# Kernel optimization log

Measured on AMD Instinct MI355X. Metric: run time of the kernel, lower is better.

The kernel has to match this reference:

```python
import jax, jax.numpy as jnp
import numpy as np

B, N_PER, C, K = 64, 2048, 512, 512


def setup_inputs() -> dict:
    key = jax.random.key(0)
    k1, k2 = jax.random.split(key)
    feat0 = jax.random.normal(k1, (B * N_PER, C, 1), dtype=jnp.float32)
    # torch.randn(1, C) / sqrt(C)
    W = jax.random.normal(k2, (1, C), dtype=jnp.float32) / np.sqrt(C).astype(np.float32)
    return {"feat0": feat0, "W": W, "num_graphs": B, "nodes_per_graph": N_PER, "k": K}


def reference(feat0, W, num_graphs, nodes_per_graph, k):
    # feat0: [N, C, 1] degree-0 features, W: [1, C] projection weights
    Cdim = feat0.shape[1]
    # yi = (W @ feat) / ||W||  ->  one scalar score per node, shape [N, 1, 1]
    y = jnp.einsum('oc,nci->noi', W, feat0) / jnp.linalg.norm(W)
    yb = y.reshape(num_graphs, nodes_per_graph)  # [B, n] per-graph scores
    # descending top-k per graph (all graphs full -> no -inf padding needed)
    _, idx = jax.lax.top_k(yb, k)                 # [B, k] unsorted positions
    idx_sorted = jnp.sort(idx, axis=1)            # torch.sort(topk_indices, dim=1)
    # selected scores, shape [B*k, 1] (hidden_size = 1)
    y_sel = jnp.take_along_axis(yb, idx_sorted, axis=1).reshape(num_graphs * k, 1)
    # flattened node indices (equivalent to topk_indices_ with hidden_size=1)
    flat_idx = (idx_sorted + jnp.arange(num_graphs)[:, None] * nodes_per_graph).reshape(-1)
    feats_sel = feat0[flat_idx].reshape(num_graphs * k, Cdim)  # gather_row on xi
    # sigmoid gate and trailing unsqueeze -> [B*k, C, 1]
    out = (jax.nn.sigmoid(y_sel) * feats_sel)[..., None]
    return out, flat_idx
```

## Files before the change

### kernel.cpp

```cpp
#include <hip/hip_runtime.h>
#include <math.h>

#define NGRAPHS 64
#define NPER    2048
#define CDIM    512
#define KSEL    512
#define NNODES  (NGRAPHS * NPER)
#define NSEL    (NGRAPHS * KSEL)
#define OUT0    (NSEL * CDIM)

__global__ void norm_kernel(const float* __restrict__ W, float* __restrict__ invnorm) {
    __shared__ float red[512];
    int t = threadIdx.x;
    float w = W[t];
    red[t] = w * w;
    __syncthreads();
    for (int s = 256; s > 0; s >>= 1) {
        if (t < s) red[t] += red[t + s];
        __syncthreads();
    }
    if (t == 0) invnorm[0] = 1.0f / sqrtf(red[0]);
}

__global__ void scores_kernel(const float* __restrict__ feat,
                              const float* __restrict__ W,
                              float* __restrict__ scores) {
    int gtid = blockIdx.x * blockDim.x + threadIdx.x;
    int row  = gtid >> 6;
    int lane = threadIdx.x & 63;
    if (row >= NNODES) return;
    const float4* rowp = (const float4*)(feat + (size_t)row * CDIM);
    const float4* Wp   = (const float4*)W;
    float acc = 0.f;
#pragma unroll
    for (int p = 0; p < 2; ++p) {
        float4 f = rowp[lane + 64 * p];
        float4 w = Wp[lane + 64 * p];
        acc += f.x * w.x + f.y * w.y + f.z * w.z + f.w * w.w;
    }
#pragma unroll
    for (int off = 32; off > 0; off >>= 1) acc += __shfl_down(acc, off);
    if (lane == 0) scores[row] = acc;
}

__global__ void __launch_bounds__(1024) topk_kernel(const float* __restrict__ scores,
                                                    int* __restrict__ flatidx,
                                                    float* __restrict__ idx_out) {
    __shared__ float s[NPER];
    __shared__ int   id[NPER];
    int b = blockIdx.x;
    int t = threadIdx.x;
    const float* sb = scores + b * NPER;
    for (int i = t; i < NPER; i += 1024) { s[i] = sb[i]; id[i] = i; }
    __syncthreads();

    for (int k = 2; k <= NPER; k <<= 1) {
        for (int j = k >> 1; j > 0; j >>= 1) {
            int i = t + (t & ~(j - 1));
            int p = i | j;
            bool up = ((i & k) == 0);
            float si = s[i], sp = s[p];
            int   ii = id[i], ip = id[p];
            bool before = (si > sp) || (si == sp && ii < ip);
            if (up ? !before : before) {
                s[i] = sp; s[p] = si; id[i] = ip; id[p] = ii;
            }
            __syncthreads();
        }
    }

    for (int k = 2; k <= KSEL; k <<= 1) {
        for (int j = k >> 1; j > 0; j >>= 1) {
            if (t < KSEL / 2) {
                int i = t + (t & ~(j - 1));
                int p = i | j;
                bool up = ((i & k) == 0);
                int ii = id[i], ip = id[p];
                if (up ? (ii > ip) : (ii < ip)) { id[i] = ip; id[p] = ii; }
            }
            __syncthreads();
        }
    }

    if (t < KSEL) {
        int fi = b * NPER + id[t];
        flatidx[b * KSEL + t] = fi;
        idx_out[b * KSEL + t] = (float)fi;
    }
}

__global__ void gather_kernel(const float* __restrict__ feat,
                              const float* __restrict__ scores,
                              const float* __restrict__ invnorm,
                              const int* __restrict__ flatidx,
                              float* __restrict__ out) {
    int gtid = blockIdx.x * blockDim.x + threadIdx.x;
    int row  = gtid >> 6;
    int lane = threadIdx.x & 63;
    if (row >= NSEL) return;
    int fi = flatidx[row];
    float y = scores[fi] * invnorm[0];
    float g = 1.0f / (1.0f + expf(-y));
    const float4* src = (const float4*)(feat + (size_t)fi * CDIM);
    float4*       dst = (float4*)(out + (size_t)row * CDIM);
#pragma unroll
    for (int p = 0; p < 2; ++p) {
        float4 f = src[lane + 64 * p];
        f.x *= g; f.y *= g; f.z *= g; f.w *= g;
        dst[lane + 64 * p] = f;
    }
}

extern "C" void kernel_launch(void* const* d_in, const int* in_sizes, int n_in,
                              void* d_out, int out_size, void* d_ws, size_t ws_size,
                              hipStream_t stream) {
    const float* feat = (const float*)d_in[0];
    const float* W    = (const float*)d_in[1];
    float* out     = (float*)d_out;
    float* idx_out = out + OUT0;

    float* ws      = (float*)d_ws;
    float* scores  = ws;
    float* invnorm = ws + NNODES;
    int*   flatidx = (int*)(ws + NNODES + 64);

    norm_kernel  <<<1, 512, 0, stream>>>(W, invnorm);
    scores_kernel<<<NNODES / 4, 256, 0, stream>>>(feat, W, scores);
    topk_kernel  <<<NGRAPHS, 1024, 0, stream>>>(scores, flatidx, idx_out);
    gather_kernel<<<NSEL / 4, 256, 0, stream>>>(feat, scores, invnorm, flatidx, out);
}
```

Before: 415.9 us.

## Replace bitonic top-k with radix threshold select and fuse norm into scoring

The per-graph full bitonic sort of 2048 scores plus the index re-sort is replaced by a 32-step radix bisection on order-preserving float keys. It finds the k-th largest threshold, then uses prefix scans to emit selected indices already in ascending index order, with ties resolved by lowest index. The W norm is now computed inside each scoring warp instead of in a separate kernel, and the sigmoid gate is computed in top-k. Gather uses nontemporal stores and all kernels use larger blocks. Each scoring warp redundantly recomputes the norm, and the radix loop still needs two block barriers per bit.

```diff
diff --git a/kernel.cpp b/kernel.cpp
--- a/kernel.cpp
+++ b/kernel.cpp
@@ -9,105 +9,130 @@
 #define NSEL    (NGRAPHS * KSEL)
 #define OUT0    (NSEL * CDIM)
 
-__global__ void norm_kernel(const float* __restrict__ W, float* __restrict__ invnorm) {
-    __shared__ float red[512];
-    int t = threadIdx.x;
-    float w = W[t];
-    red[t] = w * w;
-    __syncthreads();
-    for (int s = 256; s > 0; s >>= 1) {
-        if (t < s) red[t] += red[t + s];
-        __syncthreads();
-    }
-    if (t == 0) invnorm[0] = 1.0f / sqrtf(red[0]);
-}
+typedef float floatx4 __attribute__((ext_vector_type(4)));
 
-__global__ void scores_kernel(const float* __restrict__ feat,
-                              const float* __restrict__ W,
-                              float* __restrict__ scores) {
+__global__ void __launch_bounds__(1024) scores_kernel(const float* __restrict__ feat,
+                                                      const float* __restrict__ W,
+                                                      float* __restrict__ nscores) {
     int gtid = blockIdx.x * blockDim.x + threadIdx.x;
     int row  = gtid >> 6;
     int lane = threadIdx.x & 63;
-    if (row >= NNODES) return;
     const float4* rowp = (const float4*)(feat + (size_t)row * CDIM);
     const float4* Wp   = (const float4*)W;
-    float acc = 0.f;
+    float acc = 0.f, wss = 0.f;
 #pragma unroll
     for (int p = 0; p < 2; ++p) {
         float4 f = rowp[lane + 64 * p];
         float4 w = Wp[lane + 64 * p];
         acc += f.x * w.x + f.y * w.y + f.z * w.z + f.w * w.w;
+        wss += w.x * w.x + w.y * w.y + w.z * w.z + w.w * w.w;
     }
 #pragma unroll
-    for (int off = 32; off > 0; off >>= 1) acc += __shfl_down(acc, off);
-    if (lane == 0) scores[row] = acc;
+    for (int off = 32; off; off >>= 1) {
+        acc += __shfl_down(acc, off);
+        wss += __shfl_down(wss, off);
+    }
+    if (lane == 0) nscores[row] = acc / sqrtf(wss);
 }
 
-__global__ void __launch_bounds__(1024) topk_kernel(const float* __restrict__ scores,
-                                                    int* __restrict__ flatidx,
-                                                    float* __restrict__ idx_out) {
-    __shared__ float s[NPER];
-    __shared__ int   id[NPER];
-    int b = blockIdx.x;
-    int t = threadIdx.x;
-    const float* sb = scores + b * NPER;
-    for (int i = t; i < NPER; i += 1024) { s[i] = sb[i]; id[i] = i; }
-    __syncthreads();
+__global__ void __launch_bounds__(512) topk_kernel(const float* __restrict__ nscores,
+                                                   int* __restrict__ flatidx,
+                                                   float* __restrict__ gate,
+                                                   float* __restrict__ idx_out) {
+    int b = blockIdx.x, t = threadIdx.x;
+    int lane = t & 63, wid = t >> 6;
+    const float* sb = nscores + b * NPER;
 
-    for (int k = 2; k <= NPER; k <<= 1) {
-        for (int j = k >> 1; j > 0; j >>= 1) {
-            int i = t + (t & ~(j - 1));
-            int p = i | j;
-            bool up = ((i & k) == 0);
-            float si = s[i], sp = s[p];
-            int   ii = id[i], ip = id[p];
-            bool before = (si > sp) || (si == sp && ii < ip);
-            if (up ? !before : before) {
-                s[i] = sp; s[p] = si; id[i] = ip; id[p] = ii;
-            }
-            __syncthreads();
-        }
+    float sc[4]; unsigned key[4];
+    float4 s4 = ((const float4*)sb)[t];
+    sc[0] = s4.x; sc[1] = s4.y; sc[2] = s4.z; sc[3] = s4.w;
+#pragma unroll
+    for (int e = 0; e < 4; ++e) {
+        unsigned u = __float_as_uint(sc[e]);
+        key[e] = (u & 0x80000000u) ? ~u : (u | 0x80000000u);
     }
 
-    for (int k = 2; k <= KSEL; k <<= 1) {
-        for (int j = k >> 1; j > 0; j >>= 1) {
-            if (t < KSEL / 2) {
-                int i = t + (t & ~(j - 1));
-                int p = i | j;
-                bool up = ((i & k) == 0);
-                int ii = id[i], ip = id[p];
-                if (up ? (ii > ip) : (ii < ip)) { id[i] = ip; id[p] = ii; }
-            }
-            __syncthreads();
+    __shared__ unsigned wred[8];
+    __shared__ unsigned bc;
+    unsigned prefix = 0u;
+    for (int bit = 31; bit >= 0; --bit) {
+        unsigned cand = prefix | (1u << bit);
+        int c = (key[0] >= cand) + (key[1] >= cand) + (key[2] >= cand) + (key[3] >= cand);
+#pragma unroll
+        for (int off = 32; off; off >>= 1) c += __shfl_down(c, off);
+        if (lane == 0) wred[wid] = (unsigned)c;
+        __syncthreads();
+        if (t == 0) {
+            unsigned tot = 0;
+#pragma unroll
+            for (int w = 0; w < 8; ++w) tot += wred[w];
+            bc = tot;
         }
+        __syncthreads();
+        if (bc >= (unsigned)KSEL) prefix = cand;
     }
+    unsigned T = prefix;
 
-    if (t < KSEL) {
-        int fi = b * NPER + id[t];
-        flatidx[b * KSEL + t] = fi;
-        idx_out[b * KSEL + t] = (float)fi;
+    int gt[4], eq[4], cgt = 0, ceq = 0;
+#pragma unroll
+    for (int e = 0; e < 4; ++e) {
+        gt[e] = key[e] > T; eq[e] = key[e] == T;
+        cgt += gt[e]; ceq += eq[e];
+    }
+    int ig = cgt, ie = ceq;
+#pragma unroll
+    for (int off = 1; off < 64; off <<= 1) {
+        int ng = __shfl_up(ig, off), ne = __shfl_up(ie, off);
+        if (lane >= off) { ig += ng; ie += ne; }
+    }
+    __shared__ int wg[8], we[8], wgx[9], wex[9];
+    if (lane == 63) { wg[wid] = ig; we[wid] = ie; }
+    __syncthreads();
+    if (t == 0) {
+        int ag = 0, ae = 0;
+        for (int w = 0; w < 8; ++w) { wgx[w] = ag; wex[w] = ae; ag += wg[w]; ae += we[w]; }
+        wgx[8] = ag; wex[8] = ae;
+    }
+    __syncthreads();
+    int base_gt = wgx[wid] + ig - cgt;
+    int base_eq = wex[wid] + ie - ceq;
+    int need = KSEL - wgx[8];
+
+    int*   fo = flatidx + b * KSEL;
+    float* io = idx_out + b * KSEL;
+    float* go = gate    + b * KSEL;
+#pragma unroll
+    for (int e = 0; e < 4; ++e) {
+        int i = t * 4 + e;
+        bool sel = false; int pos = 0;
+        if (gt[e]) { sel = true; pos = base_gt + (base_eq < need ? base_eq : need); }
+        else if (eq[e] && base_eq < need) { sel = true; pos = base_gt + base_eq; }
+        if (sel) {
+            int fi = b * NPER + i;
+            fo[pos] = fi;
+            io[pos] = (float)fi;
+            go[pos] = 1.0f / (1.0f + expf(-sc[e]));
+        }
+        base_gt += gt[e]; base_eq += eq[e];
     }
 }
 
-__global__ void gather_kernel(const float* __restrict__ feat,
-                              const float* __restrict__ scores,
-                              const float* __restrict__ invnorm,
-                              const int* __restrict__ flatidx,
-                              float* __restrict__ out) {
+__global__ void __launch_bounds__(1024) gather_kernel(const float* __restrict__ feat,
+                                                      const float* __restrict__ gate,
+                                                      const int* __restrict__ flatidx,
+                                                      float* __restrict__ out) {
     int gtid = blockIdx.x * blockDim.x + threadIdx.x;
     int row  = gtid >> 6;
     int lane = threadIdx.x & 63;
-    if (row >= NSEL) return;
-    int fi = flatidx[row];
-    float y = scores[fi] * invnorm[0];
-    float g = 1.0f / (1.0f + expf(-y));
-    const float4* src = (const float4*)(feat + (size_t)fi * CDIM);
-    float4*       dst = (float4*)(out + (size_t)row * CDIM);
+    int   fi = flatidx[row];
+    float g  = gate[row];
+    const floatx4* src = (const floatx4*)(feat + (size_t)fi * CDIM);
+    floatx4*       dst = (floatx4*)(out + (size_t)row * CDIM);
 #pragma unroll
     for (int p = 0; p < 2; ++p) {
-        float4 f = src[lane + 64 * p];
-        f.x *= g; f.y *= g; f.z *= g; f.w *= g;
-        dst[lane + 64 * p] = f;
+        floatx4 f = src[lane + 64 * p];
+        f *= g;
+        __builtin_nontemporal_store(f, &dst[lane + 64 * p]);
     }
 }
 
@@ -120,12 +145,11 @@
     float* idx_out = out + OUT0;
 
     float* ws      = (float*)d_ws;
-    float* scores  = ws;
-    float* invnorm = ws + NNODES;
-    int*   flatidx = (int*)(ws + NNODES + 64);
+    float* nscores = ws;
+    float* gate    = ws + NNODES;
+    int*   flatidx = (int*)(ws + NNODES + NSEL);
 
-    norm_kernel  <<<1, 512, 0, stream>>>(W, invnorm);
-    scores_kernel<<<NNODES / 4, 256, 0, stream>>>(feat, W, scores);
-    topk_kernel  <<<NGRAPHS, 1024, 0, stream>>>(scores, flatidx, idx_out);
-    gather_kernel<<<NSEL / 4, 256, 0, stream>>>(feat, scores, invnorm, flatidx, out);
+    scores_kernel<<<NNODES * 64 / 1024, 1024, 0, stream>>>(feat, W, nscores);
+    topk_kernel  <<<NGRAPHS, 512, 0, stream>>>(nscores, flatidx, gate, idx_out);
+    gather_kernel<<<NSEL * 64 / 1024, 1024, 0, stream>>>(feat, gate, flatidx, out);
 }
```

Measured after the change: 402.5 us. 1.03x faster.
